# Optimization experiments

Measured on AMD Instinct MI355X. Metric: run time of the kernel, lower is better.

## Reference

```python
import jax, jax.numpy as jnp
import numpy as np

B, HW, L, D = 4, 4096, 32, 128
H, DH = 2, 64            # heads, dim_head; inner_dim = H*DH = 128
SCALE = DH ** -0.5


def setup_inputs() -> dict:
    key = jax.random.key(0)
    ks = jax.random.split(key, 6)
    inner = H * DH
    return {
        "x": jax.random.normal(ks[0], (B, HW, 1, D), dtype=jnp.float32),
        "context": jax.random.normal(ks[1], (B, HW, L, D), dtype=jnp.float32),
        "Wq": jax.random.normal(ks[2], (D, inner), dtype=jnp.float32) * 0.02,
        "Wkv": jax.random.normal(ks[3], (D, 2 * inner), dtype=jnp.float32) * 0.02,
        "Wo": jax.random.normal(ks[4], (inner, D), dtype=jnp.float32) * 0.02,
        "bo": jnp.zeros((D,), dtype=jnp.float32),
    }


def reference(x, context, Wq, Wkv, Wo, bo):
    # q: [B, HW, 1, H*DH] -> [B, HW, H, DH] (single query per pixel)
    q = (x @ Wq).reshape(B, HW, H, DH)
    kv = context @ Wkv                       # [B, HW, L, 2*H*DH]
    k, v = jnp.split(kv, 2, axis=-1)
    k = k.reshape(B, HW, L, H, DH)
    v = v.reshape(B, HW, L, H, DH)
    # per-pixel 1xL attention, fused over (B, HW, H)
    sim = jnp.einsum('bphd,bplhd->bphl', q, k) * SCALE   # [B, HW, H, L]
    attn = jax.nn.softmax(sim, axis=-1)
    out = jnp.einsum('bphl,bplhd->bphd', attn, v)        # [B, HW, H, DH]
    out = out.reshape(B, HW, 1, H * DH)
    return out @ Wo + bo                                 # [B, HW, 1, D]
```

## Files before the change

kernel.cpp:

```cpp
#include <hip/hip_runtime.h>

#define NPIX 16384
#define LCTX 32
#define DIM  128
#define SCALE 0.125f

__global__ __launch_bounds__(256)
void fold_kernel(const float* __restrict__ Wq, const float* __restrict__ Wkv,
                 const float* __restrict__ Wo,
                 float* __restrict__ Ms, float* __restrict__ Nf)
{
    const int t = threadIdx.x;
    const int b = blockIdx.x;
    if (b < 128) {
        const int e = b, h = t >> 7, c = t & 127;
        const float4* q4p = reinterpret_cast<const float4*>(Wq + e * 128 + h * 64);
        const float4* k4p = reinterpret_cast<const float4*>(Wkv + c * 256 + h * 64);
        float acc = 0.f;
        #pragma unroll
        for (int d4 = 0; d4 < 16; ++d4) {
            const float4 a = q4p[d4], k = k4p[d4];
            acc += a.x * k.x + a.y * k.y + a.z * k.z + a.w * k.w;
        }
        Ms[e * 256 + t] = SCALE * acc;
    } else {
        const int b2 = b - 128;
        const int i = b2 * 2 + (t >> 7), j = t & 127;
        const int h = i >> 7, c = i & 127;
        const float4* v4p = reinterpret_cast<const float4*>(Wkv + c * 256 + 128 + h * 64);
        float acc = 0.f;
        #pragma unroll
        for (int d4 = 0; d4 < 16; ++d4) {
            const float4 v4 = v4p[d4];
            acc += v4.x * Wo[(h * 64 + d4 * 4 + 0) * 128 + j];
            acc += v4.y * Wo[(h * 64 + d4 * 4 + 1) * 128 + j];
            acc += v4.z * Wo[(h * 64 + d4 * 4 + 2) * 128 + j];
            acc += v4.w * Wo[(h * 64 + d4 * 4 + 3) * 128 + j];
        }
        Nf[i * 128 + j] = acc;
    }
}

__global__ __launch_bounds__(256, 2)
void qk_kernel(const float* __restrict__ x, const float* __restrict__ Ms,
               float* __restrict__ QK)
{
    __shared__ float xs[32 * 128];
    const int t = threadIdx.x;
    const int pxbase = blockIdx.x * 32;
    #pragma unroll
    for (int k = 0; k < 4; ++k)
        reinterpret_cast<float4*>(xs)[t + k * 256] =
            reinterpret_cast<const float4*>(x + (size_t)pxbase * 128)[t + k * 256];
    __syncthreads();

    const int jq = t & 63;
    const int w  = t >> 6;
    float4 acc[8];
    #pragma unroll
    for (int pp = 0; pp < 8; ++pp) acc[pp] = make_float4(0.f, 0.f, 0.f, 0.f);

    for (int e4 = 0; e4 < 32; ++e4) {
        float4 xv[8];
        #pragma unroll
        for (int pp = 0; pp < 8; ++pp)
            xv[pp] = reinterpret_cast<const float4*>(xs + (w * 8 + pp) * 128)[e4];
        #pragma unroll
        for (int d = 0; d < 4; ++d) {
            const float4 m4 = reinterpret_cast<const float4*>(Ms + (e4 * 4 + d) * 256)[jq];
            #pragma unroll
            for (int pp = 0; pp < 8; ++pp) {
                const float xe = (d == 0) ? xv[pp].x : (d == 1) ? xv[pp].y
                               : (d == 2) ? xv[pp].z : xv[pp].w;
                acc[pp].x += xe * m4.x; acc[pp].y += xe * m4.y;
                acc[pp].z += xe * m4.z; acc[pp].w += xe * m4.w;
            }
        }
    }
    #pragma unroll
    for (int pp = 0; pp < 8; ++pp)
        reinterpret_cast<float4*>(QK + (size_t)(pxbase + w * 8 + pp) * 256)[jq] = acc[pp];
}

__global__ __launch_bounds__(256, 8)
void attn_kernel(const float* __restrict__ ctx, const float* __restrict__ QK,
                 float* __restrict__ CTXW)
{
    const int t = threadIdx.x;
    const int w = t >> 6, lane = t & 63;
    const int c0 = lane & 31;
    const int lh = lane >> 5;
    const size_t p = (size_t)blockIdx.x * 4 + w;

    const float4* cb = reinterpret_cast<const float4*>(ctx + p * LCTX * DIM);
    const float4 qh = reinterpret_cast<const float4*>(QK + p * 256)[lh * 32 + c0];

    float m = -3.0e38f, dn = 0.f;
    float4 acc = make_float4(0.f, 0.f, 0.f, 0.f);

    #pragma unroll 8
    for (int r = 0; r < LCTX; ++r) {
        const float4 cv = cb[r * 32 + c0];
        float part = cv.x * qh.x + cv.y * qh.y + cv.z * qh.z + cv.w * qh.w;
        #pragma unroll
        for (int off = 16; off >= 1; off >>= 1) part += __shfl_xor(part, off);
        const float mn = fmaxf(m, part);
        const float sc = __expf(m - mn);
        const float er = __expf(part - mn);
        dn = dn * sc + er;
        acc.x = acc.x * sc + er * cv.x;
        acc.y = acc.y * sc + er * cv.y;
        acc.z = acc.z * sc + er * cv.z;
        acc.w = acc.w * sc + er * cv.w;
        m = mn;
    }
    const float inv = 1.f / dn;
    acc.x *= inv; acc.y *= inv; acc.z *= inv; acc.w *= inv;
    reinterpret_cast<float4*>(CTXW + p * 256)[lh * 32 + c0] = acc;
}

__global__ __launch_bounds__(256, 2)
void out_kernel(const float* __restrict__ CTXW, const float* __restrict__ Nf,
                const float* __restrict__ bo, float* __restrict__ out)
{
    __shared__ float cs[32 * 256];
    const int t = threadIdx.x;
    const int pxbase = blockIdx.x * 32;
    #pragma unroll
    for (int k = 0; k < 8; ++k)
        reinterpret_cast<float4*>(cs)[t + k * 256] =
            reinterpret_cast<const float4*>(CTXW + (size_t)pxbase * 256)[t + k * 256];
    __syncthreads();

    const int lane = t & 63, w = t >> 6;
    const int jq = lane & 31;
    const int ph = lane >> 5;
    float4 acc[4];
    #pragma unroll
    for (int pp = 0; pp < 4; ++pp) acc[pp] = make_float4(0.f, 0.f, 0.f, 0.f);

    for (int i4 = 0; i4 < 64; ++i4) {
        float4 cw[4];
        #pragma unroll
        for (int pp = 0; pp < 4; ++pp)
            cw[pp] = reinterpret_cast<const float4*>(cs + (w * 8 + ph * 4 + pp) * 256)[i4];
        #pragma unroll
        for (int d = 0; d < 4; ++d) {
            const float4 n4 = reinterpret_cast<const float4*>(Nf + (i4 * 4 + d) * 128)[jq];
            #pragma unroll
            for (int pp = 0; pp < 4; ++pp) {
                const float ce = (d == 0) ? cw[pp].x : (d == 1) ? cw[pp].y
                               : (d == 2) ? cw[pp].z : cw[pp].w;
                acc[pp].x += ce * n4.x; acc[pp].y += ce * n4.y;
                acc[pp].z += ce * n4.z; acc[pp].w += ce * n4.w;
            }
        }
    }
    const float4 b4 = reinterpret_cast<const float4*>(bo)[jq];
    #pragma unroll
    for (int pp = 0; pp < 4; ++pp) {
        float4 r = acc[pp];
        r.x += b4.x; r.y += b4.y; r.z += b4.z; r.w += b4.w;
        reinterpret_cast<float4*>(out + (size_t)(pxbase + w * 8 + ph * 4 + pp) * 128)[jq] = r;
    }
}

#define PPB 8
__global__ __launch_bounds__(256, 4)
void ppca_kernel(const float* __restrict__ x, const float* __restrict__ ctx,
                 const float* __restrict__ Wq, const float* __restrict__ Wkv,
                 const float* __restrict__ Wo, const float* __restrict__ bo,
                 float* __restrict__ out)
{
    __shared__ float smem[4096];
    float* xs    = smem;
    float* qs    = smem + 1024;
    float* qks   = smem + 2048;
    float* attns = smem;
    float* ctxws = smem + 2048;
    float* outs  = smem + 1024;

    const int t = threadIdx.x;
    const int gbase = blockIdx.x * PPB;

    reinterpret_cast<float4*>(xs)[t] =
        reinterpret_cast<const float4*>(x + (size_t)gbase * DIM)[t];
    __syncthreads();

    {
        const int j = t & 127, pg = t >> 7;
        float acc[4] = {0.f, 0.f, 0.f, 0.f};
        for (int k = 0; k < 32; ++k) {
            const float w0 = Wq[(4*k + 0) * DIM + j];
            const float w1 = Wq[(4*k + 1) * DIM + j];
            const float w2 = Wq[(4*k + 2) * DIM + j];
            const float w3 = Wq[(4*k + 3) * DIM + j];
            #pragma unroll
            for (int pp = 0; pp < 4; ++pp) {
                const float4 xv = reinterpret_cast<const float4*>(xs + (pg*4 + pp) * DIM)[k];
                acc[pp] += xv.x*w0 + xv.y*w1 + xv.z*w2 + xv.w*w3;
            }
        }
        #pragma unroll
        for (int pp = 0; pp < 4; ++pp) qs[(pg*4 + pp) * DIM + j] = acc[pp];
    }
    __syncthreads();

    {
        const int c = t & 127, h = t >> 7;
        float acc[PPB] = {0.f,0.f,0.f,0.f,0.f,0.f,0.f,0.f};
        const float4* wrow = reinterpret_cast<const float4*>(Wkv + c * 256 + h * 64);
        for (int k = 0; k < 16; ++k) {
            const float4 w4 = wrow[k];
            #pragma unroll
            for (int p = 0; p < PPB; ++p) {
                const float4 q4 = reinterpret_cast<const float4*>(qs + p * DIM + h * 64)[k];
                acc[p] += q4.x*w4.x + q4.y*w4.y + q4.z*w4.z + q4.w*w4.w;
            }
        }
        #pragma unroll
        for (int p = 0; p < PPB; ++p) qks[(p*2 + h) * DIM + c] = acc[p];
    }
    __syncthreads();

    {
        const int l = t & 31, p = t >> 5;
        const float4* cr = reinterpret_cast<const float4*>(ctx + ((size_t)(gbase + p) * LCTX + l) * DIM);
        const float4* q0 = reinterpret_cast<const float4*>(qks + (p*2 + 0) * DIM);
        const float4* q1 = reinterpret_cast<const float4*>(qks + (p*2 + 1) * DIM);
        float s0 = 0.f, s1 = 0.f;
        #pragma unroll 8
        for (int k = 0; k < 32; ++k) {
            const float4 cv = cr[k], a = q0[k], b = q1[k];
            s0 += cv.x*a.x + cv.y*a.y + cv.z*a.z + cv.w*a.w;
            s1 += cv.x*b.x + cv.y*b.y + cv.z*b.z + cv.w*b.w;
        }
        s0 *= SCALE; s1 *= SCALE;
        float m0 = s0, m1 = s1;
        #pragma unroll
        for (int off = 16; off >= 1; off >>= 1) {
            m0 = fmaxf(m0, __shfl_xor(m0, off));
            m1 = fmaxf(m1, __shfl_xor(m1, off));
        }
        const float e0 = __expf(s0 - m0), e1 = __expf(s1 - m1);
        float d0 = e0, d1 = e1;
        #pragma unroll
        for (int off = 16; off >= 1; off >>= 1) {
            d0 += __shfl_xor(d0, off);
            d1 += __shfl_xor(d1, off);
        }
        attns[(p*2 + 0) * LCTX + l] = e0 / d0;
        attns[(p*2 + 1) * LCTX + l] = e1 / d1;
    }
    __syncthreads();

    {
        const int c = t & 127, pg = t >> 7;
        #pragma unroll
        for (int pp = 0; pp < 4; ++pp) {
            const int p = pg*4 + pp;
            const float* cb = ctx + (size_t)(gbase + p) * LCTX * DIM + c;
            const float4* a0p = reinterpret_cast<const float4*>(attns + (p*2 + 0) * LCTX);
            const float4* a1p = reinterpret_cast<const float4*>(attns + (p*2 + 1) * LCTX);
            float s0 = 0.f, s1 = 0.f;
            #pragma unroll
            for (int q = 0; q < 8; ++q) {
                const float4 a0 = a0p[q], a1 = a1p[q];
                const float c0 = cb[(size_t)(4*q + 0) * DIM];
                const float c1 = cb[(size_t)(4*q + 1) * DIM];
                const float c2 = cb[(size_t)(4*q + 2) * DIM];
                const float c3 = cb[(size_t)(4*q + 3) * DIM];
                s0 += a0.x*c0 + a0.y*c1 + a0.z*c2 + a0.w*c3;
                s1 += a1.x*c0 + a1.y*c1 + a1.z*c2 + a1.w*c3;
            }
            ctxws[(p*2 + 0) * DIM + c] = s0;
            ctxws[(p*2 + 1) * DIM + c] = s1;
        }
    }
    __syncthreads();

    {
        const int i = t & 127, pg = t >> 7, h = i >> 6;
        float acc[4] = {0.f, 0.f, 0.f, 0.f};
        for (int k = 0; k < 32; ++k) {
            const float w0 = Wkv[(4*k + 0) * 256 + 128 + i];
            const float w1 = Wkv[(4*k + 1) * 256 + 128 + i];
            const float w2 = Wkv[(4*k + 2) * 256 + 128 + i];
            const float w3 = Wkv[(4*k + 3) * 256 + 128 + i];
            #pragma unroll
            for (int pp = 0; pp < 4; ++pp) {
                const float4 cw = reinterpret_cast<const float4*>(ctxws + ((pg*4 + pp)*2 + h) * DIM)[k];
                acc[pp] += cw.x*w0 + cw.y*w1 + cw.z*w2 + cw.w*w3;
            }
        }
        #pragma unroll
        for (int pp = 0; pp < 4; ++pp) outs[(pg*4 + pp) * DIM + i] = acc[pp];
    }
    __syncthreads();

    {
        const int j = t & 127, pg = t >> 7;
        float acc[4] = {0.f, 0.f, 0.f, 0.f};
        for (int k = 0; k < 32; ++k) {
            const float w0 = Wo[(4*k + 0) * DIM + j];
            const float w1 = Wo[(4*k + 1) * DIM + j];
            const float w2 = Wo[(4*k + 2) * DIM + j];
            const float w3 = Wo[(4*k + 3) * DIM + j];
            #pragma unroll
            for (int pp = 0; pp < 4; ++pp) {
                const float4 ov = reinterpret_cast<const float4*>(outs + (pg*4 + pp) * DIM)[k];
                acc[pp] += ov.x*w0 + ov.y*w1 + ov.z*w2 + ov.w*w3;
            }
        }
        const float bj = bo[j];
        #pragma unroll
        for (int pp = 0; pp < 4; ++pp)
            out[(size_t)(gbase + pg*4 + pp) * DIM + j] = acc[pp] + bj;
    }
}

extern "C" void kernel_launch(void* const* d_in, const int* in_sizes, int n_in,
                              void* d_out, int out_size, void* d_ws, size_t ws_size,
                              hipStream_t stream) {
    const float* x   = (const float*)d_in[0];
    const float* ctx = (const float*)d_in[1];
    const float* Wq  = (const float*)d_in[2];
    const float* Wkv = (const float*)d_in[3];
    const float* Wo  = (const float*)d_in[4];
    const float* bo  = (const float*)d_in[5];
    float* out = (float*)d_out;

    const size_t needed = (size_t)(32768 + 32768 + 4194304 + 4194304) * sizeof(float);
    if (ws_size < needed) {
        dim3 grid(NPIX / PPB), block(256);
        hipLaunchKernelGGL(ppca_kernel, grid, block, 0, stream,
                           x, ctx, Wq, Wkv, Wo, bo, out);
        return;
    }

    float* Ms   = (float*)d_ws;
    float* Nf   = Ms + 32768;
    float* QK   = Nf + 32768;
    float* CTXW = QK + 4194304;

    hipLaunchKernelGGL(fold_kernel, dim3(256),  dim3(256), 0, stream, Wq, Wkv, Wo, Ms, Nf);
    hipLaunchKernelGGL(qk_kernel,   dim3(512),  dim3(256), 0, stream, x, Ms, QK);
    hipLaunchKernelGGL(attn_kernel, dim3(4096), dim3(256), 0, stream, ctx, QK, CTXW);
    hipLaunchKernelGGL(out_kernel,  dim3(512),  dim3(256), 0, stream, CTXW, Nf, bo, out);
}
```

Baseline: 109.1 us.

## Fuse qk projection, attention and output projection into one kernel

```diff
diff --git a/kernel.cpp b/kernel.cpp
--- a/kernel.cpp
+++ b/kernel.cpp
@@ -41,127 +41,129 @@
     }
 }
 
-__global__ __launch_bounds__(256, 2)
-void qk_kernel(const float* __restrict__ x, const float* __restrict__ Ms,
-               float* __restrict__ QK)
+__global__ __launch_bounds__(256, 4)
+void fused_kernel(const float* __restrict__ x, const float* __restrict__ ctx,
+                  const float* __restrict__ Ms, const float* __restrict__ Nf,
+                  const float* __restrict__ bo, float* __restrict__ out)
 {
-    __shared__ float xs[32 * 128];
-    const int t = threadIdx.x;
-    const int pxbase = blockIdx.x * 32;
-    #pragma unroll
-    for (int k = 0; k < 4; ++k)
-        reinterpret_cast<float4*>(xs)[t + k * 256] =
-            reinterpret_cast<const float4*>(x + (size_t)pxbase * 128)[t + k * 256];
-    __syncthreads();
-
-    const int jq = t & 63;
-    const int w  = t >> 6;
-    float4 acc[8];
-    #pragma unroll
-    for (int pp = 0; pp < 8; ++pp) acc[pp] = make_float4(0.f, 0.f, 0.f, 0.f);
-
-    for (int e4 = 0; e4 < 32; ++e4) {
-        float4 xv[8];
-        #pragma unroll
-        for (int pp = 0; pp < 8; ++pp)
-            xv[pp] = reinterpret_cast<const float4*>(xs + (w * 8 + pp) * 128)[e4];
-        #pragma unroll
-        for (int d = 0; d < 4; ++d) {
-            const float4 m4 = reinterpret_cast<const float4*>(Ms + (e4 * 4 + d) * 256)[jq];
-            #pragma unroll
-            for (int pp = 0; pp < 8; ++pp) {
-                const float xe = (d == 0) ? xv[pp].x : (d == 1) ? xv[pp].y
-                               : (d == 2) ? xv[pp].z : xv[pp].w;
-                acc[pp].x += xe * m4.x; acc[pp].y += xe * m4.y;
-                acc[pp].z += xe * m4.z; acc[pp].w += xe * m4.w;
-            }
-        }
-    }
-    #pragma unroll
-    for (int pp = 0; pp < 8; ++pp)
-        reinterpret_cast<float4*>(QK + (size_t)(pxbase + w * 8 + pp) * 256)[jq] = acc[pp];
-}
-
-__global__ __launch_bounds__(256, 8)
-void attn_kernel(const float* __restrict__ ctx, const float* __restrict__ QK,
-                 float* __restrict__ CTXW)
-{
+    __shared__ float xs[16 * 128];
+    __shared__ float cs[16 * 256];
+
     const int t = threadIdx.x;
     const int w = t >> 6, lane = t & 63;
     const int c0 = lane & 31;
     const int lh = lane >> 5;
-    const size_t p = (size_t)blockIdx.x * 4 + w;
-
-    const float4* cb = reinterpret_cast<const float4*>(ctx + p * LCTX * DIM);
-    const float4 qh = reinterpret_cast<const float4*>(QK + p * 256)[lh * 32 + c0];
-
-    float m = -3.0e38f, dn = 0.f;
-    float4 acc = make_float4(0.f, 0.f, 0.f, 0.f);
-
-    #pragma unroll 8
-    for (int r = 0; r < LCTX; ++r) {
-        const float4 cv = cb[r * 32 + c0];
-        float part = cv.x * qh.x + cv.y * qh.y + cv.z * qh.z + cv.w * qh.w;
-        #pragma unroll
-        for (int off = 16; off >= 1; off >>= 1) part += __shfl_xor(part, off);
-        const float mn = fmaxf(m, part);
-        const float sc = __expf(m - mn);
-        const float er = __expf(part - mn);
-        dn = dn * sc + er;
-        acc.x = acc.x * sc + er * cv.x;
-        acc.y = acc.y * sc + er * cv.y;
-        acc.z = acc.z * sc + er * cv.z;
-        acc.w = acc.w * sc + er * cv.w;
-        m = mn;
-    }
-    const float inv = 1.f / dn;
-    acc.x *= inv; acc.y *= inv; acc.z *= inv; acc.w *= inv;
-    reinterpret_cast<float4*>(CTXW + p * 256)[lh * 32 + c0] = acc;
-}
-
-__global__ __launch_bounds__(256, 2)
-void out_kernel(const float* __restrict__ CTXW, const float* __restrict__ Nf,
-                const float* __restrict__ bo, float* __restrict__ out)
-{
-    __shared__ float cs[32 * 256];
-    const int t = threadIdx.x;
-    const int pxbase = blockIdx.x * 32;
+    const int pxbase = blockIdx.x * 16;
+    const int wpx = pxbase + w * 4;
+
     #pragma unroll
-    for (int k = 0; k < 8; ++k)
-        reinterpret_cast<float4*>(cs)[t + k * 256] =
-            reinterpret_cast<const float4*>(CTXW + (size_t)pxbase * 256)[t + k * 256];
-    __syncthreads();
-
-    const int lane = t & 63, w = t >> 6;
-    const int jq = lane & 31;
-    const int ph = lane >> 5;
+    for (int k = 0; k < 2; ++k)
+        reinterpret_cast<float4*>(xs)[t + k * 256] =
+            reinterpret_cast<const float4*>(x + (size_t)pxbase * DIM)[t + k * 256];
+    __syncthreads();
+
+    float4 qk4[4];
+    #pragma unroll
+    for (int p = 0; p < 4; ++p) qk4[p] = make_float4(0.f, 0.f, 0.f, 0.f);
+    {
+        const float4* ms4 = reinterpret_cast<const float4*>(Ms) + (lh * 32 + c0);
+        const float4* xw  = reinterpret_cast<const float4*>(xs + (w * 4) * DIM);
+        for (int e4 = 0; e4 < 32; ++e4) {
+            float4 xv[4];
+            #pragma unroll
+            for (int p = 0; p < 4; ++p) xv[p] = xw[p * 32 + e4];
+            #pragma unroll
+            for (int d = 0; d < 4; ++d) {
+                const float4 m4 = ms4[(e4 * 4 + d) * 64];
+                #pragma unroll
+                for (int p = 0; p < 4; ++p) {
+                    const float xe = (d == 0) ? xv[p].x : (d == 1) ? xv[p].y
+                                   : (d == 2) ? xv[p].z : xv[p].w;
+                    qk4[p].x += xe * m4.x; qk4[p].y += xe * m4.y;
+                    qk4[p].z += xe * m4.z; qk4[p].w += xe * m4.w;
+                }
+            }
+        }
+    }
+
+    float m[4], dn[4];
     float4 acc[4];
     #pragma unroll
-    for (int pp = 0; pp < 4; ++pp) acc[pp] = make_float4(0.f, 0.f, 0.f, 0.f);
-
-    for (int i4 = 0; i4 < 64; ++i4) {
-        float4 cw[4];
-        #pragma unroll
-        for (int pp = 0; pp < 4; ++pp)
-            cw[pp] = reinterpret_cast<const float4*>(cs + (w * 8 + ph * 4 + pp) * 256)[i4];
-        #pragma unroll
-        for (int d = 0; d < 4; ++d) {
-            const float4 n4 = reinterpret_cast<const float4*>(Nf + (i4 * 4 + d) * 128)[jq];
-            #pragma unroll
-            for (int pp = 0; pp < 4; ++pp) {
-                const float ce = (d == 0) ? cw[pp].x : (d == 1) ? cw[pp].y
-                               : (d == 2) ? cw[pp].z : cw[pp].w;
-                acc[pp].x += ce * n4.x; acc[pp].y += ce * n4.y;
-                acc[pp].z += ce * n4.z; acc[pp].w += ce * n4.w;
-            }
-        }
-    }
-    const float4 b4 = reinterpret_cast<const float4*>(bo)[jq];
-    #pragma unroll
-    for (int pp = 0; pp < 4; ++pp) {
-        float4 r = acc[pp];
-        r.x += b4.x; r.y += b4.y; r.z += b4.z; r.w += b4.w;
-        reinterpret_cast<float4*>(out + (size_t)(pxbase + w * 8 + ph * 4 + pp) * 128)[jq] = r;
+    for (int p = 0; p < 4; ++p) {
+        m[p] = -3.0e38f; dn[p] = 0.f;
+        acc[p] = make_float4(0.f, 0.f, 0.f, 0.f);
+    }
+    {
+        const float4* cb0 = reinterpret_cast<const float4*>(ctx + (size_t)(wpx + 0) * LCTX * DIM) + c0;
+        const float4* cb1 = reinterpret_cast<const float4*>(ctx + (size_t)(wpx + 1) * LCTX * DIM) + c0;
+        const float4* cb2 = reinterpret_cast<const float4*>(ctx + (size_t)(wpx + 2) * LCTX * DIM) + c0;
+        const float4* cb3 = reinterpret_cast<const float4*>(ctx + (size_t)(wpx + 3) * LCTX * DIM) + c0;
+        #pragma unroll 4
+        for (int r = 0; r < LCTX; ++r) {
+            float4 cv[4];
+            cv[0] = cb0[r * 32]; cv[1] = cb1[r * 32];
+            cv[2] = cb2[r * 32]; cv[3] = cb3[r * 32];
+            float part[4];
+            #pragma unroll
+            for (int p = 0; p < 4; ++p)
+                part[p] = cv[p].x * qk4[p].x + cv[p].y * qk4[p].y
+                        + cv[p].z * qk4[p].z + cv[p].w * qk4[p].w;
+            #pragma unroll
+            for (int off = 16; off >= 1; off >>= 1) {
+                #pragma unroll
+                for (int p = 0; p < 4; ++p) part[p] += __shfl_xor(part[p], off);
+            }
+            #pragma unroll
+            for (int p = 0; p < 4; ++p) {
+                const float mn = fmaxf(m[p], part[p]);
+                const float sc = __expf(m[p] - mn);
+                const float er = __expf(part[p] - mn);
+                dn[p] = dn[p] * sc + er;
+                acc[p].x = acc[p].x * sc + er * cv[p].x;
+                acc[p].y = acc[p].y * sc + er * cv[p].y;
+                acc[p].z = acc[p].z * sc + er * cv[p].z;
+                acc[p].w = acc[p].w * sc + er * cv[p].w;
+                m[p] = mn;
+            }
+        }
+    }
+    {
+        float* csw = cs + (w * 4) * 256;
+        #pragma unroll
+        for (int p = 0; p < 4; ++p) {
+            const float inv = 1.f / dn[p];
+            float4 r = acc[p];
+            r.x *= inv; r.y *= inv; r.z *= inv; r.w *= inv;
+            reinterpret_cast<float4*>(csw + p * 256)[lh * 32 + c0] = r;
+        }
+    }
+
+    {
+        const int jq = lane & 31;
+        const int ph = lane >> 5;
+        const float4* csv0 = reinterpret_cast<const float4*>(cs + (w * 4 + ph * 2 + 0) * 256);
+        const float4* csv1 = reinterpret_cast<const float4*>(cs + (w * 4 + ph * 2 + 1) * 256);
+        const float4* nf4 = reinterpret_cast<const float4*>(Nf) + jq;
+        float4 o0 = make_float4(0.f, 0.f, 0.f, 0.f);
+        float4 o1 = make_float4(0.f, 0.f, 0.f, 0.f);
+        #pragma unroll 4
+        for (int i4 = 0; i4 < 64; ++i4) {
+            const float4 a0 = csv0[i4];
+            const float4 a1 = csv1[i4];
+            #pragma unroll
+            for (int d = 0; d < 4; ++d) {
+                const float4 n4 = nf4[(i4 * 4 + d) * 32];
+                const float a0e = (d == 0) ? a0.x : (d == 1) ? a0.y : (d == 2) ? a0.z : a0.w;
+                const float a1e = (d == 0) ? a1.x : (d == 1) ? a1.y : (d == 2) ? a1.z : a1.w;
+                o0.x += a0e * n4.x; o0.y += a0e * n4.y; o0.z += a0e * n4.z; o0.w += a0e * n4.w;
+                o1.x += a1e * n4.x; o1.y += a1e * n4.y; o1.z += a1e * n4.z; o1.w += a1e * n4.w;
+            }
+        }
+        const float4 b4 = reinterpret_cast<const float4*>(bo)[jq];
+        o0.x += b4.x; o0.y += b4.y; o0.z += b4.z; o0.w += b4.w;
+        o1.x += b4.x; o1.y += b4.y; o1.z += b4.z; o1.w += b4.w;
+        reinterpret_cast<float4*>(out + (size_t)(wpx + ph * 2 + 0) * DIM)[jq] = o0;
+        reinterpret_cast<float4*>(out + (size_t)(wpx + ph * 2 + 1) * DIM)[jq] = o1;
     }
 }
 
@@ -330,7 +332,7 @@
     const float* bo  = (const float*)d_in[5];
     float* out = (float*)d_out;
 
-    const size_t needed = (size_t)(32768 + 32768 + 4194304 + 4194304) * sizeof(float);
+    const size_t needed = (size_t)(32768 + 32768) * sizeof(float);
     if (ws_size < needed) {
         dim3 grid(NPIX / PPB), block(256);
         hipLaunchKernelGGL(ppca_kernel, grid, block, 0, stream,
@@ -338,13 +340,10 @@
         return;
     }
 
-    float* Ms   = (float*)d_ws;
-    float* Nf   = Ms + 32768;
-    float* QK   = Nf + 32768;
-    float* CTXW = QK + 4194304;
-
-    hipLaunchKernelGGL(fold_kernel, dim3(256),  dim3(256), 0, stream, Wq, Wkv, Wo, Ms, Nf);
-    hipLaunchKernelGGL(qk_kernel,   dim3(512),  dim3(256), 0, stream, x, Ms, QK);
-    hipLaunchKernelGGL(attn_kernel, dim3(4096), dim3(256), 0, stream, ctx, QK, CTXW);
-    hipLaunchKernelGGL(out_kernel,  dim3(512),  dim3(256), 0, stream, CTXW, Nf, bo, out);
+    float* Ms = (float*)d_ws;
+    float* Nf = Ms + 32768;
+
+    hipLaunchKernelGGL(fold_kernel,  dim3(256),  dim3(256), 0, stream, Wq, Wkv, Wo, Ms, Nf);
+    hipLaunchKernelGGL(fused_kernel, dim3(NPIX / 16), dim3(256), 0, stream,
+                       x, ctx, Ms, Nf, bo, out);
 }
```

New measurement: 117.5 us. +7.7%, slower.
